# Kernel optimization log

Hardware: AMD Instinct MI355X
Metric: run time of the kernel (lower is better)

The kernel has to match this reference:

```python
import jax, jax.numpy as jnp
import numpy as np

N_NODES = 50000
N_EDGES = 800000
D = 256


def gcn_conv(x, edge_index, W, b, n_nodes):
    """PyG-style GCNConv: add self-loops, symmetric norm, linear, scatter-add."""
    # add self loops
    loops = jnp.arange(n_nodes, dtype=edge_index.dtype)
    src = jnp.concatenate([edge_index[0], loops])  # message sources
    dst = jnp.concatenate([edge_index[1], loops])  # aggregation targets
    # symmetric normalization: deg computed on targets (incl. self loops)
    deg = jax.ops.segment_sum(jnp.ones_like(dst, dtype=x.dtype), dst,
                              num_segments=n_nodes)
    dinv = jnp.where(deg > 0, jax.lax.rsqrt(deg), 0.0)
    norm = dinv[src] * dinv[dst]  # [E+N]
    h = x @ W  # [N, out]
    msg = h[src] * norm[:, None]  # gather + scale, [E+N, out]
    out = jax.ops.segment_sum(msg, dst, num_segments=n_nodes)  # scatter-add
    return out + b


def setup_inputs() -> dict:
    key = jax.random.key(0)
    k1, k2, k3, k4 = jax.random.split(key, 4)
    x = jax.random.normal(k1, (N_NODES, D), dtype=jnp.float32)
    edge_index = jax.random.randint(k2, (2, N_EDGES), 0, N_NODES, dtype=jnp.int64)
    s = 1.0 / np.sqrt(D)
    W1 = jax.random.normal(k3, (D, D), dtype=jnp.float32) * s
    W2 = jax.random.normal(k4, (D, D), dtype=jnp.float32) * s
    b1 = jnp.zeros((D,), dtype=jnp.float32)
    b2 = jnp.zeros((D,), dtype=jnp.float32)
    return {"x": x, "edge_index": edge_index, "W1": W1, "b1": b1,
            "W2": W2, "b2": b2}


def reference(x, edge_index, W1, b1, W2, b2):
    n = x.shape[0]
    out = gcn_conv(x, edge_index, W1, b1, n)
    out = jax.nn.relu(out)  # dropout is identity in eval mode (p=0.2 in train)
    out = out + gcn_conv(x, edge_index, W2, b2, n)
    return out
```

## Files before the change

kernel.cpp:

```cpp
#include <hip/hip_runtime.h>
#include <hip/hip_bf16.h>

#define DIM 256
#define CAP 64
#define GEMM_BX 64

typedef short bf16x8 __attribute__((ext_vector_type(8)));
typedef float f32x4  __attribute__((ext_vector_type(4)));
typedef unsigned int u32x4 __attribute__((ext_vector_type(4)));

__device__ __forceinline__ unsigned short f2b(float f) {
    union { __hip_bfloat16 h; unsigned short u; } cv;
    cv.h = __float2bfloat16(f);
    return cv.u;
}
__device__ __forceinline__ void acc8(u32x4 u, float* a) {
    a[0] += __uint_as_float(u.x << 16); a[1] += __uint_as_float(u.x & 0xffff0000u);
    a[2] += __uint_as_float(u.y << 16); a[3] += __uint_as_float(u.y & 0xffff0000u);
    a[4] += __uint_as_float(u.z << 16); a[5] += __uint_as_float(u.z & 0xffff0000u);
    a[6] += __uint_as_float(u.w << 16); a[7] += __uint_as_float(u.w & 0xffff0000u);
}

#define OFF_FILL   0
#define OFF_WT1    262144
#define OFF_WT2    393216
#define OFF_BUCKET 524288
#define OFF_AGG    6924544ull
#define OFF_YB     32524544ull
#define NEED_BF    (OFF_YB + 25600000ull)

__global__ void k_fill(const int* __restrict__ src, const int* __restrict__ dst,
                       int* __restrict__ fill, unsigned short* __restrict__ bucket, int nE) {
    int e = blockIdx.x * blockDim.x + threadIdx.x;
    if (e < nE) {
        int d = dst[e];
        int pos = atomicAdd(&fill[d], 1);
        if (pos < CAP) bucket[d * CAP + pos] = (unsigned short)src[e];
    }
}

__global__ void k_prep(const float* __restrict__ x, const int* __restrict__ fill,
                       u32x4* __restrict__ yb,
                       const float* __restrict__ W1, const float* __restrict__ W2,
                       unsigned short* __restrict__ wt1, unsigned short* __restrict__ wt2,
                       int nybBlocks, int n8) {
    if ((int)blockIdx.x < nybBlocks) {
        int t = blockIdx.x * 256 + threadIdx.x;
        if (t < n8) {
            int nN   = n8 >> 5;
            int s    = t / (nN * 4);
            int rest = t - s * (nN * 4);
            int node = rest >> 2;
            int ch   = rest & 3;
            int g    = s * 4 + ch;
            float d = rsqrtf((float)(1 + fill[node]));
            const f32x4* xp = (const f32x4*)x + ((size_t)node * 32 + g) * 2;
            f32x4 v0 = xp[0], v1 = xp[1];
            u32x4 r;
            r.x = (unsigned)f2b(d * v0.x) | ((unsigned)f2b(d * v0.y) << 16);
            r.y = (unsigned)f2b(d * v0.z) | ((unsigned)f2b(d * v0.w) << 16);
            r.z = (unsigned)f2b(d * v1.x) | ((unsigned)f2b(d * v1.y) << 16);
            r.w = (unsigned)f2b(d * v1.z) | ((unsigned)f2b(d * v1.w) << 16);
            yb[t] = r;
        }
    } else {
        int t = (blockIdx.x - nybBlocks) * 256 + threadIdx.x;
        if (t < DIM * DIM) {
            int k = t & 255, nn = t >> 8;
            wt1[t] = f2b(W1[k * DIM + nn]);
            wt2[t] = f2b(W2[k * DIM + nn]);
        }
    }
}

__launch_bounds__(256, 4)
__global__ void k_agg_bf(const u32x4* __restrict__ yb, const int* __restrict__ fill,
                         const unsigned short* __restrict__ bucket,
                         u32x4* __restrict__ aggbf, int n) {
    int slice = blockIdx.x & 7;
    int nb    = blockIdx.x >> 3;
    int tid   = threadIdx.x;
    int grp   = tid >> 2;
    int ch    = tid & 3;
    int node  = nb * 64 + grp;
    if (node >= n) return;

    const u32x4* ybs = yb + (size_t)slice * n * 4;

    int c = __builtin_nontemporal_load(&fill[node]);
    float di = rsqrtf((float)(1 + c));
    if (c > CAP) c = CAP;
    const unsigned short* bk = bucket + (size_t)node * CAP;

    float a[8];
#pragma unroll
    for (int i = 0; i < 8; i++) a[i] = 0.f;
    acc8(ybs[node * 4 + ch], a);

#define EXTRACT8(iv, j) \
    int j##0 = iv.x & 0xffff, j##1 = iv.x >> 16, j##2 = iv.y & 0xffff, j##3 = iv.y >> 16, \
        j##4 = iv.z & 0xffff, j##5 = iv.z >> 16, j##6 = iv.w & 0xffff, j##7 = iv.w >> 16

    int full = c & ~7;
    if (full) {
        u32x4 g[8], h[8];
        u32x4 iv0 = *(const u32x4*)bk;
        {
            EXTRACT8(iv0, q);
            g[0] = ybs[q0 * 4 + ch]; g[1] = ybs[q1 * 4 + ch];
            g[2] = ybs[q2 * 4 + ch]; g[3] = ybs[q3 * 4 + ch];
            g[4] = ybs[q4 * 4 + ch]; g[5] = ybs[q5 * 4 + ch];
            g[6] = ybs[q6 * 4 + ch]; g[7] = ybs[q7 * 4 + ch];
        }
        u32x4 iv1 = *(const u32x4*)(bk + ((8 < full) ? 8 : 0));
        for (int k = 8; k < full; k += 8) {
            u32x4 ivn = *(const u32x4*)(bk + ((k + 8 < full) ? k + 8 : 0));
            {
                EXTRACT8(iv1, q);
                h[0] = ybs[q0 * 4 + ch]; h[1] = ybs[q1 * 4 + ch];
                h[2] = ybs[q2 * 4 + ch]; h[3] = ybs[q3 * 4 + ch];
                h[4] = ybs[q4 * 4 + ch]; h[5] = ybs[q5 * 4 + ch];
                h[6] = ybs[q6 * 4 + ch]; h[7] = ybs[q7 * 4 + ch];
            }
#pragma unroll
            for (int i = 0; i < 8; i++) acc8(g[i], a);
#pragma unroll
            for (int i = 0; i < 8; i++) g[i] = h[i];
            iv1 = ivn;
        }
#pragma unroll
        for (int i = 0; i < 8; i++) acc8(g[i], a);
    }

    int rem = c - full;
    if (rem) {
        u32x4 iv = *(const u32x4*)(bk + full);
        EXTRACT8(iv, q);
        q1 = (rem > 1) ? q1 : 0;
        q2 = (rem > 2) ? q2 : 0;
        q3 = (rem > 3) ? q3 : 0;
        q4 = (rem > 4) ? q4 : 0;
        q5 = (rem > 5) ? q5 : 0;
        q6 = (rem > 6) ? q6 : 0;
        u32x4 r0 = ybs[q0 * 4 + ch];
        u32x4 r1 = ybs[q1 * 4 + ch];
        u32x4 r2 = ybs[q2 * 4 + ch];
        u32x4 r3 = ybs[q3 * 4 + ch];
        u32x4 r4 = ybs[q4 * 4 + ch];
        u32x4 r5 = ybs[q5 * 4 + ch];
        u32x4 r6 = ybs[q6 * 4 + ch];
        acc8(r0, a);
        if (rem > 1) acc8(r1, a);
        if (rem > 2) acc8(r2, a);
        if (rem > 3) acc8(r3, a);
        if (rem > 4) acc8(r4, a);
        if (rem > 5) acc8(r5, a);
        if (rem > 6) acc8(r6, a);
    }
#undef EXTRACT8

    u32x4 r;
    r.x = (unsigned)f2b(a[0] * di) | ((unsigned)f2b(a[1] * di) << 16);
    r.y = (unsigned)f2b(a[2] * di) | ((unsigned)f2b(a[3] * di) << 16);
    r.z = (unsigned)f2b(a[4] * di) | ((unsigned)f2b(a[5] * di) << 16);
    r.w = (unsigned)f2b(a[6] * di) | ((unsigned)f2b(a[7] * di) << 16);
    __builtin_nontemporal_store(r, &aggbf[(size_t)node * 32 + slice * 4 + ch]);
}

__global__ void k_agg_f32(const float4* __restrict__ x4, const int* __restrict__ fill,
                          const unsigned short* __restrict__ bucket,
                          ushort4* __restrict__ aggbf, int n) {
    int node = (blockIdx.x * blockDim.x + threadIdx.x) >> 6;
    int lane = threadIdx.x & 63;
    if (node >= n) return;

    int c = fill[node];
    float di = rsqrtf((float)(1 + c));
    if (c > CAP) c = CAP;

    float4 xi = x4[(size_t)node * 64 + lane];
    float a0 = di * xi.x, a1 = di * xi.y, a2 = di * xi.z, a3 = di * xi.w;

    const unsigned short* bk = bucket + (size_t)node * CAP;
    for (int k = 0; k < c; k++) {
        int j = bk[k];
        float dj = rsqrtf((float)(1 + fill[j]));
        float4 xj = x4[(size_t)j * 64 + lane];
        a0 += dj * xj.x; a1 += dj * xj.y; a2 += dj * xj.z; a3 += dj * xj.w;
    }
    ushort4 r;
    r.x = f2b(a0 * di); r.y = f2b(a1 * di);
    r.z = f2b(a2 * di); r.w = f2b(a3 * di);
    aggbf[(size_t)node * 64 + lane] = r;
}

__launch_bounds__(256, 2)
__global__ void k_gemm(const short* __restrict__ aggbf,
                       const short* __restrict__ wt1, const short* __restrict__ wt2,
                       const float* __restrict__ b1, const float* __restrict__ b2,
                       float* __restrict__ out, int n, int ntiles) {
    __shared__ u32x4 bs[2048];

    int c0  = blockIdx.y * 32;
    int tid = threadIdx.x;

#pragma unroll
    for (int i = 0; i < 8; i++) {
        int l = tid + i * 256;
        int m = l >> 10, rem = l & 1023, nn = rem >> 5, p = rem & 31;
        const short* base = (m == 0) ? wt1 : wt2;
        const u32x4* sp = (const u32x4*)(base + (size_t)(c0 + nn) * DIM) + p;
        bs[(m << 10) + (nn << 5) + (p ^ nn)] = *sp;
    }
    __syncthreads();

    int lane = tid & 63;
    int wave = tid >> 6;
    int lrow = lane & 15;
    int quad = lane >> 4;

    bf16x8 w1r[2][8], w2r[2][8];
#pragma unroll
    for (int ct = 0; ct < 2; ct++) {
        int nn = ct * 16 + lrow;
#pragma unroll
        for (int s = 0; s < 8; s++) {
            int p = (4 * s + quad) ^ nn;
            u32x4 u = bs[(nn << 5) + p];
            u32x4 v = bs[1024 + (nn << 5) + p];
            __builtin_memcpy(&w1r[ct][s], &u, 16);
            __builtin_memcpy(&w2r[ct][s], &v, 16);
        }
    }

    f32x4 bb1[2], bb2[2];
#pragma unroll
    for (int ct = 0; ct < 2; ct++) {
        bb1[ct] = *(const f32x4*)&b1[c0 + ct * 16 + quad * 4];
        bb2[ct] = *(const f32x4*)&b2[c0 + ct * 16 + quad * 4];
    }

    for (int t = blockIdx.x; t < ntiles; t += gridDim.x) {
        int row = t * 64 + wave * 16 + lrow;
        int r = (row < n) ? row : 0;
        const short* ap = aggbf + (size_t)r * DIM + quad * 8;

        bf16x8 A[8];
#pragma unroll
        for (int s = 0; s < 8; s++) A[s] = *(const bf16x8*)(ap + s * 32);

        f32x4 acc1[2], acc2[2];
#pragma unroll
        for (int ct = 0; ct < 2; ct++) {
            acc1[ct] = (f32x4){0.f, 0.f, 0.f, 0.f};
            acc2[ct] = (f32x4){0.f, 0.f, 0.f, 0.f};
        }

#pragma unroll
        for (int s = 0; s < 8; s++) {
#pragma unroll
            for (int ct = 0; ct < 2; ct++) {
                acc1[ct] = __builtin_amdgcn_mfma_f32_16x16x32_bf16(w1r[ct][s], A[s], acc1[ct], 0, 0, 0);
                acc2[ct] = __builtin_amdgcn_mfma_f32_16x16x32_bf16(w2r[ct][s], A[s], acc2[ct], 0, 0, 0);
            }
        }

        if (row < n) {
#pragma unroll
            for (int ct = 0; ct < 2; ct++) {
                f32x4 v;
#pragma unroll
                for (int i = 0; i < 4; i++)
                    v[i] = fmaxf(acc1[ct][i] + bb1[ct][i], 0.f) + acc2[ct][i] + bb2[ct][i];
                f32x4* dstp = (f32x4*)&out[(size_t)row * DIM + c0 + ct * 16 + quad * 4];
                __builtin_nontemporal_store(v, dstp);
            }
        }
    }
}

extern "C" void kernel_launch(void* const* d_in, const int* in_sizes, int n_in,
                              void* d_out, int out_size, void* d_ws, size_t ws_size,
                              hipStream_t stream) {
    const float* x  = (const float*)d_in[0];
    const int*   ei = (const int*)d_in[1];
    const float* W1 = (const float*)d_in[2];
    const float* b1 = (const float*)d_in[3];
    const float* W2 = (const float*)d_in[4];
    const float* b2 = (const float*)d_in[5];
    float* out = (float*)d_out;

    int n = in_sizes[0] / DIM;
    int E = in_sizes[1] / 2;
    const int* src = ei;
    const int* dst = ei + E;

    char* ws = (char*)d_ws;
    int*            fill   = (int*)(ws + OFF_FILL);
    unsigned short* wt1    = (unsigned short*)(ws + OFF_WT1);
    unsigned short* wt2    = (unsigned short*)(ws + OFF_WT2);
    unsigned short* bucket = (unsigned short*)(ws + OFF_BUCKET);
    char*           aggp   = ws + OFF_AGG;
    u32x4*          yb     = (u32x4*)(ws + OFF_YB);

    (void)hipMemsetAsync(fill, 0, n * sizeof(int), stream);

    k_fill<<<(E + 255) / 256, 256, 0, stream>>>(src, dst, fill, bucket, E);

    bool use_bf = (ws_size >= NEED_BF);
    if (use_bf) {
        int n8 = n * (DIM / 8);
        int nybBlocks = (n8 + 255) / 256;
        k_prep<<<nybBlocks + 256, 256, 0, stream>>>(x, fill, yb, W1, W2, wt1, wt2,
                                                    nybBlocks, n8);
        int aggBlocks = ((n + 63) / 64) * 8;
        k_agg_bf<<<aggBlocks, 256, 0, stream>>>(yb, fill, bucket, (u32x4*)aggp, n);
    } else {
        k_prep<<<256, 256, 0, stream>>>(x, fill, yb, W1, W2, wt1, wt2, 0, 0);
        int aggBlocks = (n * 64 + 255) / 256;
        k_agg_f32<<<aggBlocks, 256, 0, stream>>>((const float4*)x, fill, bucket,
                                                 (ushort4*)aggp, n);
    }

    int ntiles = (n + 63) / 64;
    dim3 ggrid(GEMM_BX, DIM / 32);
    k_gemm<<<ggrid, 256, 0, stream>>>((const short*)aggp, (const short*)wt1,
                                      (const short*)wt2, b1, b2, out, n, ntiles);
}
```

Baseline: 239.2 us.

## Fuse edge bucketing with bf16 conversion and apply source degree norm in aggregation

The edge-bucketing pass and the x-to-bf16 conversion now run in one kernel with interleaved blocks, so the conversion no longer waits for the degree counts. The source-side normalization moves out of the conversion into the aggregation, which applies it per neighbour with an FMA using a precomputed dinv array built by a small new kernel. The goal is to overlap the atomic bucketing with the streaming conversion and drop one dependency. The cost is an extra scalar gather of dinv per neighbour, one more kernel launch, and larger workspace needs that could turn off the bf16 path.

```diff
diff --git a/kernel.cpp b/kernel.cpp
--- a/kernel.cpp
+++ b/kernel.cpp
@@ -14,11 +14,15 @@
     cv.h = __float2bfloat16(f);
     return cv.u;
 }
-__device__ __forceinline__ void acc8(u32x4 u, float* a) {
-    a[0] += __uint_as_float(u.x << 16); a[1] += __uint_as_float(u.x & 0xffff0000u);
-    a[2] += __uint_as_float(u.y << 16); a[3] += __uint_as_float(u.y & 0xffff0000u);
-    a[4] += __uint_as_float(u.z << 16); a[5] += __uint_as_float(u.z & 0xffff0000u);
-    a[6] += __uint_as_float(u.w << 16); a[7] += __uint_as_float(u.w & 0xffff0000u);
+__device__ __forceinline__ void facc8(u32x4 u, float f, float* a) {
+    a[0] = fmaf(__uint_as_float(u.x << 16), f, a[0]);
+    a[1] = fmaf(__uint_as_float(u.x & 0xffff0000u), f, a[1]);
+    a[2] = fmaf(__uint_as_float(u.y << 16), f, a[2]);
+    a[3] = fmaf(__uint_as_float(u.y & 0xffff0000u), f, a[3]);
+    a[4] = fmaf(__uint_as_float(u.z << 16), f, a[4]);
+    a[5] = fmaf(__uint_as_float(u.z & 0xffff0000u), f, a[5]);
+    a[6] = fmaf(__uint_as_float(u.w << 16), f, a[6]);
+    a[7] = fmaf(__uint_as_float(u.w & 0xffff0000u), f, a[7]);
 }
 
 #define OFF_FILL   0
@@ -27,44 +31,46 @@
 #define OFF_BUCKET 524288
 #define OFF_AGG    6924544ull
 #define OFF_YB     32524544ull
-#define NEED_BF    (OFF_YB + 25600000ull)
-
-__global__ void k_fill(const int* __restrict__ src, const int* __restrict__ dst,
-                       int* __restrict__ fill, unsigned short* __restrict__ bucket, int nE) {
-    int e = blockIdx.x * blockDim.x + threadIdx.x;
-    if (e < nE) {
-        int d = dst[e];
-        int pos = atomicAdd(&fill[d], 1);
-        if (pos < CAP) bucket[d * CAP + pos] = (unsigned short)src[e];
-    }
-}
-
-__global__ void k_prep(const float* __restrict__ x, const int* __restrict__ fill,
-                       u32x4* __restrict__ yb,
-                       const float* __restrict__ W1, const float* __restrict__ W2,
-                       unsigned short* __restrict__ wt1, unsigned short* __restrict__ wt2,
-                       int nybBlocks, int n8) {
-    if ((int)blockIdx.x < nybBlocks) {
-        int t = blockIdx.x * 256 + threadIdx.x;
-        if (t < n8) {
-            int nN   = n8 >> 5;
-            int s    = t / (nN * 4);
-            int rest = t - s * (nN * 4);
-            int node = rest >> 2;
-            int ch   = rest & 3;
-            int g    = s * 4 + ch;
-            float d = rsqrtf((float)(1 + fill[node]));
-            const f32x4* xp = (const f32x4*)x + ((size_t)node * 32 + g) * 2;
-            f32x4 v0 = xp[0], v1 = xp[1];
-            u32x4 r;
-            r.x = (unsigned)f2b(d * v0.x) | ((unsigned)f2b(d * v0.y) << 16);
-            r.y = (unsigned)f2b(d * v0.z) | ((unsigned)f2b(d * v0.w) << 16);
-            r.z = (unsigned)f2b(d * v1.x) | ((unsigned)f2b(d * v1.y) << 16);
-            r.w = (unsigned)f2b(d * v1.z) | ((unsigned)f2b(d * v1.w) << 16);
-            yb[t] = r;
+#define OFF_DINV   58124544ull
+#define NEED_BF    (OFF_DINV + 200704ull)
+
+__global__ void k_fillprep(const int* __restrict__ src, const int* __restrict__ dst,
+                           int* __restrict__ fill, unsigned short* __restrict__ bucket,
+                           const float* __restrict__ x, u32x4* __restrict__ yb,
+                           const float* __restrict__ W1, const float* __restrict__ W2,
+                           unsigned short* __restrict__ wt1, unsigned short* __restrict__ wt2,
+                           int base3, int nE, int n8) {
+    int bid = blockIdx.x;
+    if (bid < base3) {
+        int b3 = bid / 3, r = bid - b3 * 3;
+        if (r == 0) {
+            int e = b3 * 256 + threadIdx.x;
+            if (e < nE) {
+                int d = dst[e];
+                int pos = atomicAdd(&fill[d], 1);
+                if (pos < CAP) bucket[d * CAP + pos] = (unsigned short)src[e];
+            }
+        } else {
+            int t = (2 * b3 + r - 1) * 256 + threadIdx.x;
+            if (t < n8) {
+                int nN   = n8 >> 5;
+                int s    = t / (nN * 4);
+                int rest = t - s * (nN * 4);
+                int node = rest >> 2;
+                int ch   = rest & 3;
+                int g    = s * 4 + ch;
+                const f32x4* xp = (const f32x4*)x + ((size_t)node * 32 + g) * 2;
+                f32x4 v0 = xp[0], v1 = xp[1];
+                u32x4 rr;
+                rr.x = (unsigned)f2b(v0.x) | ((unsigned)f2b(v0.y) << 16);
+                rr.y = (unsigned)f2b(v0.z) | ((unsigned)f2b(v0.w) << 16);
+                rr.z = (unsigned)f2b(v1.x) | ((unsigned)f2b(v1.y) << 16);
+                rr.w = (unsigned)f2b(v1.z) | ((unsigned)f2b(v1.w) << 16);
+                yb[t] = rr;
+            }
         }
     } else {
-        int t = (blockIdx.x - nybBlocks) * 256 + threadIdx.x;
+        int t = (bid - base3) * 256 + threadIdx.x;
         if (t < DIM * DIM) {
             int k = t & 255, nn = t >> 8;
             wt1[t] = f2b(W1[k * DIM + nn]);
@@ -73,8 +79,14 @@
     }
 }
 
+__global__ void k_dinv(const int* __restrict__ fill, float* __restrict__ dinv, int n) {
+    int i = blockIdx.x * 256 + threadIdx.x;
+    if (i < n) dinv[i] = rsqrtf((float)(1 + fill[i]));
+}
+
 __launch_bounds__(256, 4)
 __global__ void k_agg_bf(const u32x4* __restrict__ yb, const int* __restrict__ fill,
+                         const float* __restrict__ dinv,
                          const unsigned short* __restrict__ bucket,
                          u32x4* __restrict__ aggbf, int n) {
     int slice = blockIdx.x & 7;
@@ -87,15 +99,15 @@
 
     const u32x4* ybs = yb + (size_t)slice * n * 4;
 
+    float di = dinv[node];
     int c = __builtin_nontemporal_load(&fill[node]);
-    float di = rsqrtf((float)(1 + c));
     if (c > CAP) c = CAP;
     const unsigned short* bk = bucket + (size_t)node * CAP;
 
     float a[8];
 #pragma unroll
     for (int i = 0; i < 8; i++) a[i] = 0.f;
-    acc8(ybs[node * 4 + ch], a);
+    facc8(ybs[(size_t)node * 4 + ch], di, a);
 
 #define EXTRACT8(iv, j) \
     int j##0 = iv.x & 0xffff, j##1 = iv.x >> 16, j##2 = iv.y & 0xffff, j##3 = iv.y >> 16, \
@@ -104,6 +116,7 @@
     int full = c & ~7;
     if (full) {
         u32x4 g[8], h[8];
+        float dg[8], dh[8];
         u32x4 iv0 = *(const u32x4*)bk;
         {
             EXTRACT8(iv0, q);
@@ -111,6 +124,8 @@
             g[2] = ybs[q2 * 4 + ch]; g[3] = ybs[q3 * 4 + ch];
             g[4] = ybs[q4 * 4 + ch]; g[5] = ybs[q5 * 4 + ch];
             g[6] = ybs[q6 * 4 + ch]; g[7] = ybs[q7 * 4 + ch];
+            dg[0] = dinv[q0]; dg[1] = dinv[q1]; dg[2] = dinv[q2]; dg[3] = dinv[q3];
+            dg[4] = dinv[q4]; dg[5] = dinv[q5]; dg[6] = dinv[q6]; dg[7] = dinv[q7];
         }
         u32x4 iv1 = *(const u32x4*)(bk + ((8 < full) ? 8 : 0));
         for (int k = 8; k < full; k += 8) {
@@ -121,15 +136,17 @@
                 h[2] = ybs[q2 * 4 + ch]; h[3] = ybs[q3 * 4 + ch];
                 h[4] = ybs[q4 * 4 + ch]; h[5] = ybs[q5 * 4 + ch];
                 h[6] = ybs[q6 * 4 + ch]; h[7] = ybs[q7 * 4 + ch];
-            }
-#pragma unroll
-            for (int i = 0; i < 8; i++) acc8(g[i], a);
-#pragma unroll
-            for (int i = 0; i < 8; i++) g[i] = h[i];
+                dh[0] = dinv[q0]; dh[1] = dinv[q1]; dh[2] = dinv[q2]; dh[3] = dinv[q3];
+                dh[4] = dinv[q4]; dh[5] = dinv[q5]; dh[6] = dinv[q6]; dh[7] = dinv[q7];
+            }
+#pragma unroll
+            for (int i = 0; i < 8; i++) facc8(g[i], dg[i], a);
+#pragma unroll
+            for (int i = 0; i < 8; i++) { g[i] = h[i]; dg[i] = dh[i]; }
             iv1 = ivn;
         }
 #pragma unroll
-        for (int i = 0; i < 8; i++) acc8(g[i], a);
+        for (int i = 0; i < 8; i++) facc8(g[i], dg[i], a);
     }
 
     int rem = c - full;
@@ -149,13 +166,15 @@
         u32x4 r4 = ybs[q4 * 4 + ch];
         u32x4 r5 = ybs[q5 * 4 + ch];
         u32x4 r6 = ybs[q6 * 4 + ch];
-        acc8(r0, a);
-        if (rem > 1) acc8(r1, a);
-        if (rem > 2) acc8(r2, a);
-        if (rem > 3) acc8(r3, a);
-        if (rem > 4) acc8(r4, a);
-        if (rem > 5) acc8(r5, a);
-        if (rem > 6) acc8(r6, a);
+        float d0 = dinv[q0], d1 = dinv[q1], d2 = dinv[q2], d3 = dinv[q3];
+        float d4 = dinv[q4], d5 = dinv[q5], d6 = dinv[q6];
+        facc8(r0, d0, a);
+        if (rem > 1) facc8(r1, d1, a);
+        if (rem > 2) facc8(r2, d2, a);
+        if (rem > 3) facc8(r3, d3, a);
+        if (rem > 4) facc8(r4, d4, a);
+        if (rem > 5) facc8(r5, d5, a);
+        if (rem > 6) facc8(r6, d6, a);
     }
 #undef EXTRACT8
 
@@ -302,21 +321,27 @@
     unsigned short* bucket = (unsigned short*)(ws + OFF_BUCKET);
     char*           aggp   = ws + OFF_AGG;
     u32x4*          yb     = (u32x4*)(ws + OFF_YB);
+    float*          dinv   = (float*)(ws + OFF_DINV);
 
     (void)hipMemsetAsync(fill, 0, n * sizeof(int), stream);
 
-    k_fill<<<(E + 255) / 256, 256, 0, stream>>>(src, dst, fill, bucket, E);
-
+    int nFillBlocks = (E + 255) / 256;
     bool use_bf = (ws_size >= NEED_BF);
     if (use_bf) {
         int n8 = n * (DIM / 8);
-        int nybBlocks = (n8 + 255) / 256;
-        k_prep<<<nybBlocks + 256, 256, 0, stream>>>(x, fill, yb, W1, W2, wt1, wt2,
-                                                    nybBlocks, n8);
+        int ybBlocks = (n8 + 255) / 256;
+        int base = nFillBlocks > (ybBlocks + 1) / 2 ? nFillBlocks : (ybBlocks + 1) / 2;
+        k_fillprep<<<base * 3 + 256, 256, 0, stream>>>(src, dst, fill, bucket,
+                                                       x, yb, W1, W2, wt1, wt2,
+                                                       base * 3, E, n8);
+        k_dinv<<<(n + 255) / 256, 256, 0, stream>>>(fill, dinv, n);
         int aggBlocks = ((n + 63) / 64) * 8;
-        k_agg_bf<<<aggBlocks, 256, 0, stream>>>(yb, fill, bucket, (u32x4*)aggp, n);
+        k_agg_bf<<<aggBlocks, 256, 0, stream>>>(yb, fill, dinv, bucket,
+                                                (u32x4*)aggp, n);
     } else {
-        k_prep<<<256, 256, 0, stream>>>(x, fill, yb, W1, W2, wt1, wt2, 0, 0);
+        k_fillprep<<<nFillBlocks * 3 + 256, 256, 0, stream>>>(src, dst, fill, bucket,
+                                                              x, yb, W1, W2, wt1, wt2,
+                                                              nFillBlocks * 3, E, 0);
         int aggBlocks = (n * 64 + 255) / 256;
         k_agg_f32<<<aggBlocks, 256, 0, stream>>>((const float4*)x, fill, bucket,
                                                  (ushort4*)aggp, n);
```

New measurement: 254.9 us. 6.6% more time.

## Fuse memset, fill, prep and aggregation into one cooperative persistent kernel

Applied to the files above, without the earlier changes.

Replaces the memset plus three separate launches (fill, prep, aggregation) with a single cooperative kernel that runs each phase as a grid-stride loop separated by grid.sync(). This removes the launch gaps and tail effects between small kernels. In exchange it adds grid-wide barrier cost and caps aggregation parallelism at occupancy-limited persistent blocks. If the cooperative launch fails, it falls back to the old multi-kernel path.

```diff
diff --git a/kernel.cpp b/kernel.cpp
--- a/kernel.cpp
+++ b/kernel.cpp
@@ -1,5 +1,8 @@
 #include <hip/hip_runtime.h>
+#include <hip/hip_cooperative_groups.h>
 #include <hip/hip_bf16.h>
+
+namespace cg = cooperative_groups;
 
 #define DIM 256
 #define CAP 64
@@ -29,64 +32,40 @@
 #define OFF_YB     32524544ull
 #define NEED_BF    (OFF_YB + 25600000ull)
 
-__global__ void k_fill(const int* __restrict__ src, const int* __restrict__ dst,
-                       int* __restrict__ fill, unsigned short* __restrict__ bucket, int nE) {
-    int e = blockIdx.x * blockDim.x + threadIdx.x;
-    if (e < nE) {
-        int d = dst[e];
-        int pos = atomicAdd(&fill[d], 1);
-        if (pos < CAP) bucket[d * CAP + pos] = (unsigned short)src[e];
-    }
-}
-
-__global__ void k_prep(const float* __restrict__ x, const int* __restrict__ fill,
-                       u32x4* __restrict__ yb,
-                       const float* __restrict__ W1, const float* __restrict__ W2,
-                       unsigned short* __restrict__ wt1, unsigned short* __restrict__ wt2,
-                       int nybBlocks, int n8) {
-    if ((int)blockIdx.x < nybBlocks) {
-        int t = blockIdx.x * 256 + threadIdx.x;
-        if (t < n8) {
-            int nN   = n8 >> 5;
-            int s    = t / (nN * 4);
-            int rest = t - s * (nN * 4);
-            int node = rest >> 2;
-            int ch   = rest & 3;
-            int g    = s * 4 + ch;
-            float d = rsqrtf((float)(1 + fill[node]));
-            const f32x4* xp = (const f32x4*)x + ((size_t)node * 32 + g) * 2;
-            f32x4 v0 = xp[0], v1 = xp[1];
-            u32x4 r;
-            r.x = (unsigned)f2b(d * v0.x) | ((unsigned)f2b(d * v0.y) << 16);
-            r.y = (unsigned)f2b(d * v0.z) | ((unsigned)f2b(d * v0.w) << 16);
-            r.z = (unsigned)f2b(d * v1.x) | ((unsigned)f2b(d * v1.y) << 16);
-            r.w = (unsigned)f2b(d * v1.z) | ((unsigned)f2b(d * v1.w) << 16);
-            yb[t] = r;
-        }
-    } else {
-        int t = (blockIdx.x - nybBlocks) * 256 + threadIdx.x;
-        if (t < DIM * DIM) {
-            int k = t & 255, nn = t >> 8;
-            wt1[t] = f2b(W1[k * DIM + nn]);
-            wt2[t] = f2b(W2[k * DIM + nn]);
-        }
-    }
-}
-
-__launch_bounds__(256, 4)
-__global__ void k_agg_bf(const u32x4* __restrict__ yb, const int* __restrict__ fill,
-                         const unsigned short* __restrict__ bucket,
-                         u32x4* __restrict__ aggbf, int n) {
-    int slice = blockIdx.x & 7;
-    int nb    = blockIdx.x >> 3;
-    int tid   = threadIdx.x;
-    int grp   = tid >> 2;
-    int ch    = tid & 3;
-    int node  = nb * 64 + grp;
-    if (node >= n) return;
-
-    const u32x4* ybs = yb + (size_t)slice * n * 4;
-
+__device__ __forceinline__ void wt_one(int t, const float* __restrict__ W1,
+                                       const float* __restrict__ W2,
+                                       unsigned short* __restrict__ wt1,
+                                       unsigned short* __restrict__ wt2) {
+    int k = t & 255, nn = t >> 8;
+    wt1[t] = f2b(W1[k * DIM + nn]);
+    wt2[t] = f2b(W2[k * DIM + nn]);
+}
+
+__device__ __forceinline__ void yb_one(int t, int n, const int* __restrict__ fill,
+                                       const float* __restrict__ x,
+                                       u32x4* __restrict__ yb) {
+    int nN4  = n * 4;
+    int s    = t / nN4;
+    int rest = t - s * nN4;
+    int node = rest >> 2;
+    int ch   = rest & 3;
+    int g    = s * 4 + ch;
+    float d = rsqrtf((float)(1 + fill[node]));
+    const f32x4* xp = (const f32x4*)x + ((size_t)node * 64 + g * 2);
+    f32x4 v0 = xp[0], v1 = xp[1];
+    u32x4 rr;
+    rr.x = (unsigned)f2b(d * v0.x) | ((unsigned)f2b(d * v0.y) << 16);
+    rr.y = (unsigned)f2b(d * v0.z) | ((unsigned)f2b(d * v0.w) << 16);
+    rr.z = (unsigned)f2b(d * v1.x) | ((unsigned)f2b(d * v1.y) << 16);
+    rr.w = (unsigned)f2b(d * v1.z) | ((unsigned)f2b(d * v1.w) << 16);
+    yb[t] = rr;
+}
+
+__device__ __forceinline__ void agg_one(const u32x4* __restrict__ ybs,
+                                        const int* __restrict__ fill,
+                                        const unsigned short* __restrict__ bucket,
+                                        u32x4* __restrict__ aggbf,
+                                        int n, int node, int ch, int slice) {
     int c = __builtin_nontemporal_load(&fill[node]);
     float di = rsqrtf((float)(1 + c));
     if (c > CAP) c = CAP;
@@ -95,7 +74,7 @@
     float a[8];
 #pragma unroll
     for (int i = 0; i < 8; i++) a[i] = 0.f;
-    acc8(ybs[node * 4 + ch], a);
+    acc8(ybs[(size_t)node * 4 + ch], a);
 
 #define EXTRACT8(iv, j) \
     int j##0 = iv.x & 0xffff, j##1 = iv.x >> 16, j##2 = iv.y & 0xffff, j##3 = iv.y >> 16, \
@@ -167,6 +146,106 @@
     __builtin_nontemporal_store(r, &aggbf[(size_t)node * 32 + slice * 4 + ch]);
 }
 
+__launch_bounds__(256, 4)
+__global__ void k_mega(const int* __restrict__ src, const int* __restrict__ dst,
+                       int* __restrict__ fill, unsigned short* __restrict__ bucket,
+                       const float* __restrict__ x, u32x4* __restrict__ yb,
+                       const float* __restrict__ W1, const float* __restrict__ W2,
+                       unsigned short* __restrict__ wt1, unsigned short* __restrict__ wt2,
+                       u32x4* __restrict__ aggbf, int n, int E) {
+    cg::grid_group grid = cg::this_grid();
+    const int bid  = blockIdx.x;
+    const int nblk = gridDim.x;
+    const int tid  = threadIdx.x;
+    const int n8   = n * 32;
+
+    {
+        int zfB = (n + 255) >> 8;
+        int totalA = zfB + 256;
+        for (int v = bid; v < totalA; v += nblk) {
+            if (v < zfB) {
+                int i = v * 256 + tid;
+                if (i < n) fill[i] = 0;
+            } else {
+                wt_one((v - zfB) * 256 + tid, W1, W2, wt1, wt2);
+            }
+        }
+    }
+    grid.sync();
+
+    {
+        int fB = (E + 255) >> 8;
+        for (int v = bid; v < fB; v += nblk) {
+            int e = v * 256 + tid;
+            if (e < E) {
+                int d = dst[e];
+                int pos = atomicAdd(&fill[d], 1);
+                if (pos < CAP) bucket[d * CAP + pos] = (unsigned short)src[e];
+            }
+        }
+    }
+    grid.sync();
+
+    {
+        int ybB = (n8 + 255) >> 8;
+        for (int v = bid; v < ybB; v += nblk) {
+            int t = v * 256 + tid;
+            if (t < n8) yb_one(t, n, fill, x, yb);
+        }
+    }
+    grid.sync();
+
+    {
+        int slice = bid & 7;
+        const u32x4* ybs = yb + (size_t)slice * n * 4;
+        int grp = tid >> 2;
+        int ch  = tid & 3;
+        int nbTot = (n + 63) >> 6;
+        for (int nb = bid >> 3; nb < nbTot; nb += nblk >> 3) {
+            int node = nb * 64 + grp;
+            if (node < n) agg_one(ybs, fill, bucket, aggbf, n, node, ch, slice);
+        }
+    }
+}
+
+__global__ void k_fill(const int* __restrict__ src, const int* __restrict__ dst,
+                       int* __restrict__ fill, unsigned short* __restrict__ bucket, int nE) {
+    int e = blockIdx.x * blockDim.x + threadIdx.x;
+    if (e < nE) {
+        int d = dst[e];
+        int pos = atomicAdd(&fill[d], 1);
+        if (pos < CAP) bucket[d * CAP + pos] = (unsigned short)src[e];
+    }
+}
+
+__global__ void k_prep(const float* __restrict__ x, const int* __restrict__ fill,
+                       u32x4* __restrict__ yb,
+                       const float* __restrict__ W1, const float* __restrict__ W2,
+                       unsigned short* __restrict__ wt1, unsigned short* __restrict__ wt2,
+                       int nybBlocks, int n8, int n) {
+    if ((int)blockIdx.x < nybBlocks) {
+        int t = blockIdx.x * 256 + threadIdx.x;
+        if (t < n8) yb_one(t, n, fill, x, yb);
+    } else {
+        int t = (blockIdx.x - nybBlocks) * 256 + threadIdx.x;
+        if (t < DIM * DIM) wt_one(t, W1, W2, wt1, wt2);
+    }
+}
+
+__launch_bounds__(256, 4)
+__global__ void k_agg_bf(const u32x4* __restrict__ yb, const int* __restrict__ fill,
+                         const unsigned short* __restrict__ bucket,
+                         u32x4* __restrict__ aggbf, int n) {
+    int slice = blockIdx.x & 7;
+    int nb    = blockIdx.x >> 3;
+    int grp   = threadIdx.x >> 2;
+    int ch    = threadIdx.x & 3;
+    int node  = nb * 64 + grp;
+    if (node >= n) return;
+    const u32x4* ybs = yb + (size_t)slice * n * 4;
+    agg_one(ybs, fill, bucket, aggbf, n, node, ch, slice);
+}
+
 __global__ void k_agg_f32(const float4* __restrict__ x4, const int* __restrict__ fill,
                           const unsigned short* __restrict__ bucket,
                           ushort4* __restrict__ aggbf, int n) {
@@ -303,23 +382,47 @@
     char*           aggp   = ws + OFF_AGG;
     u32x4*          yb     = (u32x4*)(ws + OFF_YB);
 
-    (void)hipMemsetAsync(fill, 0, n * sizeof(int), stream);
-
-    k_fill<<<(E + 255) / 256, 256, 0, stream>>>(src, dst, fill, bucket, E);
-
     bool use_bf = (ws_size >= NEED_BF);
+
     if (use_bf) {
-        int n8 = n * (DIM / 8);
-        int nybBlocks = (n8 + 255) / 256;
-        k_prep<<<nybBlocks + 256, 256, 0, stream>>>(x, fill, yb, W1, W2, wt1, wt2,
-                                                    nybBlocks, n8);
-        int aggBlocks = ((n + 63) / 64) * 8;
-        k_agg_bf<<<aggBlocks, 256, 0, stream>>>(yb, fill, bucket, (u32x4*)aggp, n);
+        static int coopMode = 0;
+        static int gridBlocks = 0;
+        if (coopMode >= 0) {
+            if (gridBlocks == 0) {
+                int mb = 0;
+                if (hipOccupancyMaxActiveBlocksPerMultiprocessor(&mb, k_mega, 256, 0)
+                        != hipSuccess || mb < 2) mb = 2;
+                if (mb > 8) mb = 8;
+                gridBlocks = mb * 256;
+            }
+            u32x4* aggp4 = (u32x4*)aggp;
+            void* args[] = {(void*)&src, (void*)&dst, (void*)&fill, (void*)&bucket,
+                            (void*)&x, (void*)&yb, (void*)&W1, (void*)&W2,
+                            (void*)&wt1, (void*)&wt2, (void*)&aggp4,
+                            (void*)&n, (void*)&E};
+            hipError_t err = hipLaunchCooperativeKernel((void*)k_mega,
+                                                        dim3(gridBlocks), dim3(256),
+                                                        args, 0, stream);
+            coopMode = (err == hipSuccess) ? 1 : -1;
+        }
+        if (coopMode < 0) {
+            (void)hipMemsetAsync(fill, 0, n * sizeof(int), stream);
+            k_fill<<<(E + 255) / 256, 256, 0, stream>>>(src, dst, fill, bucket, E);
+            int n8 = n * 32;
+            int nybBlocks = (n8 + 255) / 256;
+            k_prep<<<nybBlocks + 256, 256, 0, stream>>>(x, fill, yb, W1, W2,
+                                                        wt1, wt2, nybBlocks, n8, n);
+            int aggBlocks = ((n + 63) / 64) * 8;
+            k_agg_bf<<<aggBlocks, 256, 0, stream>>>(yb, fill, bucket,
+                                                    (u32x4*)aggp, n);
+        }
     } else {
-        k_prep<<<256, 256, 0, stream>>>(x, fill, yb, W1, W2, wt1, wt2, 0, 0);
+        (void)hipMemsetAsync(fill, 0, n * sizeof(int), stream);
+        k_fill<<<(E + 255) / 256, 256, 0, stream>>>(src, dst, fill, bucket, E);
         int aggBlocks = (n * 64 + 255) / 256;
         k_agg_f32<<<aggBlocks, 256, 0, stream>>>((const float4*)x, fill, bucket,
                                                  (ushort4*)aggp, n);
+        k_prep<<<256, 256, 0, stream>>>(x, fill, yb, W1, W2, wt1, wt2, 0, 0, n);
     }
 
     int ntiles = (n + 63) / 64;
```

Result: slower. 448.5 us (+87.5%).

## Sort nodes into degree buckets so aggregation wavefronts see uniform degrees

Applied to the files above, without the earlier changes.

A single extra block in the prep kernel builds a histogram of per-node in-degree in buckets of 8, then scatters node ids into a permutation ordered by degree bucket. The bf16 aggregation kernel maps each thread group to perm[idx] instead of the raw node index, so lanes in a wavefront handle nodes with similar edge counts and spend less time waiting on the slowest lane. The cost is a serial single-block pass over all nodes, which may lengthen the prep kernel, and less contiguous access to node rows and outputs. The workspace requirement also grows, so a smaller workspace would push execution onto the slower f32 fallback.

```diff
diff --git a/kernel.cpp b/kernel.cpp
--- a/kernel.cpp
+++ b/kernel.cpp
@@ -27,7 +27,8 @@
 #define OFF_BUCKET 524288
 #define OFF_AGG    6924544ull
 #define OFF_YB     32524544ull
-#define NEED_BF    (OFF_YB + 25600000ull)
+#define OFF_PERM   58124544ull
+#define NEED_BF    (OFF_PERM + 131072ull)
 
 __global__ void k_fill(const int* __restrict__ src, const int* __restrict__ dst,
                        int* __restrict__ fill, unsigned short* __restrict__ bucket, int nE) {
@@ -39,51 +40,88 @@
     }
 }
 
+__device__ __forceinline__ void wt_one(int t, const float* __restrict__ W1,
+                                       const float* __restrict__ W2,
+                                       unsigned short* __restrict__ wt1,
+                                       unsigned short* __restrict__ wt2) {
+    int k = t & 255, nn = t >> 8;
+    wt1[t] = f2b(W1[k * DIM + nn]);
+    wt2[t] = f2b(W2[k * DIM + nn]);
+}
+
+__device__ __forceinline__ void yb_one(int t, int n, const int* __restrict__ fill,
+                                       const float* __restrict__ x,
+                                       u32x4* __restrict__ yb) {
+    int nN4  = n * 4;
+    int s    = t / nN4;
+    int rest = t - s * nN4;
+    int node = rest >> 2;
+    int ch   = rest & 3;
+    int g    = s * 4 + ch;
+    float d = rsqrtf((float)(1 + fill[node]));
+    const f32x4* xp = (const f32x4*)x + ((size_t)node * 64 + g * 2);
+    f32x4 v0 = xp[0], v1 = xp[1];
+    u32x4 rr;
+    rr.x = (unsigned)f2b(d * v0.x) | ((unsigned)f2b(d * v0.y) << 16);
+    rr.y = (unsigned)f2b(d * v0.z) | ((unsigned)f2b(d * v0.w) << 16);
+    rr.z = (unsigned)f2b(d * v1.x) | ((unsigned)f2b(d * v1.y) << 16);
+    rr.w = (unsigned)f2b(d * v1.z) | ((unsigned)f2b(d * v1.w) << 16);
+    yb[t] = rr;
+}
+
 __global__ void k_prep(const float* __restrict__ x, const int* __restrict__ fill,
                        u32x4* __restrict__ yb,
                        const float* __restrict__ W1, const float* __restrict__ W2,
                        unsigned short* __restrict__ wt1, unsigned short* __restrict__ wt2,
-                       int nybBlocks, int n8) {
-    if ((int)blockIdx.x < nybBlocks) {
-        int t = blockIdx.x * 256 + threadIdx.x;
-        if (t < n8) {
-            int nN   = n8 >> 5;
-            int s    = t / (nN * 4);
-            int rest = t - s * (nN * 4);
-            int node = rest >> 2;
-            int ch   = rest & 3;
-            int g    = s * 4 + ch;
-            float d = rsqrtf((float)(1 + fill[node]));
-            const f32x4* xp = (const f32x4*)x + ((size_t)node * 32 + g) * 2;
-            f32x4 v0 = xp[0], v1 = xp[1];
-            u32x4 r;
-            r.x = (unsigned)f2b(d * v0.x) | ((unsigned)f2b(d * v0.y) << 16);
-            r.y = (unsigned)f2b(d * v0.z) | ((unsigned)f2b(d * v0.w) << 16);
-            r.z = (unsigned)f2b(d * v1.x) | ((unsigned)f2b(d * v1.y) << 16);
-            r.w = (unsigned)f2b(d * v1.z) | ((unsigned)f2b(d * v1.w) << 16);
-            yb[t] = r;
-        }
+                       unsigned short* __restrict__ perm,
+                       int permB, int nybBlocks, int n8, int n) {
+    int bid = blockIdx.x;
+    if (bid < permB) {
+        __shared__ int hist[4][16];
+        __shared__ int offs[4][16];
+        int tid = threadIdx.x;
+        int w = tid >> 6;
+        if (tid < 64) hist[tid >> 4][tid & 15] = 0;
+        __syncthreads();
+        for (int i = tid; i < n; i += 256) {
+            int c = fill[i];
+            int b = (c + 7) >> 3; if (b > 15) b = 15;
+            atomicAdd(&hist[w][b], 1);
+        }
+        __syncthreads();
+        if (tid == 0) {
+            int s = 0;
+            for (int b = 0; b < 16; b++)
+                for (int ww = 0; ww < 4; ww++) { offs[ww][b] = s; s += hist[ww][b]; }
+        }
+        __syncthreads();
+        for (int i = tid; i < n; i += 256) {
+            int c = fill[i];
+            int b = (c + 7) >> 3; if (b > 15) b = 15;
+            int p = atomicAdd(&offs[w][b], 1);
+            perm[p] = (unsigned short)i;
+        }
+    } else if (bid < permB + nybBlocks) {
+        int t = (bid - permB) * 256 + threadIdx.x;
+        if (t < n8) yb_one(t, n, fill, x, yb);
     } else {
-        int t = (blockIdx.x - nybBlocks) * 256 + threadIdx.x;
-        if (t < DIM * DIM) {
-            int k = t & 255, nn = t >> 8;
-            wt1[t] = f2b(W1[k * DIM + nn]);
-            wt2[t] = f2b(W2[k * DIM + nn]);
-        }
+        int t = (bid - permB - nybBlocks) * 256 + threadIdx.x;
+        if (t < DIM * DIM) wt_one(t, W1, W2, wt1, wt2);
     }
 }
 
 __launch_bounds__(256, 4)
 __global__ void k_agg_bf(const u32x4* __restrict__ yb, const int* __restrict__ fill,
                          const unsigned short* __restrict__ bucket,
+                         const unsigned short* __restrict__ perm,
                          u32x4* __restrict__ aggbf, int n) {
     int slice = blockIdx.x & 7;
     int nb    = blockIdx.x >> 3;
-    int tid   = threadIdx.x;
-    int grp   = tid >> 2;
-    int ch    = tid & 3;
-    int node  = nb * 64 + grp;
-    if (node >= n) return;
+    int grp   = threadIdx.x >> 2;
+    int ch    = threadIdx.x & 3;
+    int idx   = nb * 64 + grp;
+    if (idx >= n) return;
+    int node  = perm[idx];
 
     const u32x4* ybs = yb + (size_t)slice * n * 4;
 
@@ -95,7 +133,7 @@
     float a[8];
 #pragma unroll
     for (int i = 0; i < 8; i++) a[i] = 0.f;
-    acc8(ybs[node * 4 + ch], a);
+    acc8(ybs[(size_t)node * 4 + ch], a);
 
 #define EXTRACT8(iv, j) \
     int j##0 = iv.x & 0xffff, j##1 = iv.x >> 16, j##2 = iv.y & 0xffff, j##3 = iv.y >> 16, \
@@ -302,6 +340,7 @@
     unsigned short* bucket = (unsigned short*)(ws + OFF_BUCKET);
     char*           aggp   = ws + OFF_AGG;
     u32x4*          yb     = (u32x4*)(ws + OFF_YB);
+    unsigned short* perm   = (unsigned short*)(ws + OFF_PERM);
 
     (void)hipMemsetAsync(fill, 0, n * sizeof(int), stream);
 
@@ -309,14 +348,17 @@
 
     bool use_bf = (ws_size >= NEED_BF);
     if (use_bf) {
-        int n8 = n * (DIM / 8);
+        int n8 = n * 32;
         int nybBlocks = (n8 + 255) / 256;
-        k_prep<<<nybBlocks + 256, 256, 0, stream>>>(x, fill, yb, W1, W2, wt1, wt2,
-                                                    nybBlocks, n8);
+        k_prep<<<1 + nybBlocks + 256, 256, 0, stream>>>(x, fill, yb, W1, W2,
+                                                        wt1, wt2, perm,
+                                                        1, nybBlocks, n8, n);
         int aggBlocks = ((n + 63) / 64) * 8;
-        k_agg_bf<<<aggBlocks, 256, 0, stream>>>(yb, fill, bucket, (u32x4*)aggp, n);
+        k_agg_bf<<<aggBlocks, 256, 0, stream>>>(yb, fill, bucket, perm,
+                                                (u32x4*)aggp, n);
     } else {
-        k_prep<<<256, 256, 0, stream>>>(x, fill, yb, W1, W2, wt1, wt2, 0, 0);
+        k_prep<<<256, 256, 0, stream>>>(x, fill, yb, W1, W2, wt1, wt2, perm,
+                                        0, 0, 0, n);
         int aggBlocks = (n * 64 + 255) / 256;
         k_agg_f32<<<aggBlocks, 256, 0, stream>>>((const float4*)x, fill, bucket,
                                                  (ushort4*)aggp, n);
```

Result: slower. 332.9 us (+39.2%).
